# Optimization experiments

Measured on AMD Instinct MI355X. Metric: run time of the kernel, lower is better.

Reference implementation:

```python
import jax, jax.numpy as jnp
import numpy as np

B, P, D, V = 8192, 32, 128, 100000  # batch, max path len, embed dim, label_num


def setup_inputs() -> dict:
    key = jax.random.key(0)
    k1, k2, k3, k4, k5, k6 = jax.random.split(key, 6)
    return {
        "hidden_": jax.random.normal(k1, (B, D), dtype=jnp.float32),
        "target": jax.random.randint(k2, (B,), 0, V, dtype=jnp.int64),
        "target_path": jax.random.randint(k3, (B, P), 0, V, dtype=jnp.int64),
        "target_path_len": jax.random.randint(k4, (B,), 1, P, dtype=jnp.int64),
        "target_code": jax.random.randint(k5, (B, P), 0, 2, dtype=jnp.int64),
        "embed_table": jax.random.normal(k6, (V, D), dtype=jnp.float32) * 0.02,
    }


def reference(hidden_, target, target_path, target_path_len, target_code, embed_table):
    # embeds: [B, P, D] gather of tree-node vectors along each label's path
    embeds = embed_table[target_path]
    # per-node score: sigmoid(<node_vec, hidden>) -> [B, P]
    score = jax.nn.sigmoid(jnp.einsum("bpd,bd->bp", embeds, hidden_))
    flag = target_code.astype(jnp.float32)
    # BCE-style per-node loss, exactly as the TF code writes it
    loss = -jnp.log(flag * score + (1.0 - flag) * (1.0 - score))
    # ragged path mask: positions < target_path_len are valid (tf.ragged.range + batch_gather)
    mask = (jnp.arange(P)[None, :] < target_path_len[:, None]).astype(jnp.float32)
    # reduce_mean over the ragged tensor = sum of valid losses / total valid count
    return jnp.sum(loss * mask) / jnp.sum(mask)
```

## Files before the change

### kernel.cpp

```cpp
#include <hip/hip_runtime.h>

#define BB 8192
#define PP 32
#define DD 128

__global__ __launch_bounds__(256) void hs_loss_kernel(
    const float* __restrict__ hidden,
    const int*   __restrict__ path,
    const int*   __restrict__ path_len,
    const int*   __restrict__ code,
    const float* __restrict__ embed,
    float2* __restrict__ partials)
{
    const int tid = threadIdx.x;
    const int b   = blockIdx.x;
    const int hw  = tid >> 5;
    const int hl  = tid & 31;
    const int p0  = hw * 4;

    const int len = path_len[b];

    float acc = 0.0f;
    if (p0 < len) {
        const int4 idx4 = ((const int4*)(path + b * PP))[hw];
        const int4 cd4  = ((const int4*)(code + b * PP))[hw];
        const float4 h  = ((const float4*)(hidden + (size_t)b * DD))[hl];

        const int nv = min(len - p0, 4);
        const int idx[4] = {idx4.x, idx4.y, idx4.z, idx4.w};
        const int cd[4]  = {cd4.x, cd4.y, cd4.z, cd4.w};

        float4 e[4];
        #pragma unroll
        for (int j = 0; j < 4; ++j)
            if (j < nv) e[j] = ((const float4*)(embed + (size_t)idx[j] * DD))[hl];

        #pragma unroll
        for (int j = 0; j < 4; ++j) {
            if (j < nv) {
                float dot = h.x * e[j].x + h.y * e[j].y + h.z * e[j].z + h.w * e[j].w;
                dot += __shfl_xor(dot, 1);
                dot += __shfl_xor(dot, 2);
                dot += __shfl_xor(dot, 4);
                dot += __shfl_xor(dot, 8);
                dot += __shfl_xor(dot, 16);
                const float z = cd[j] ? -dot : dot;
                acc += fmaxf(z, 0.0f) + log1pf(__expf(-fabsf(z)));
            }
        }
    }

    __shared__ float s_loss[8];
    if (hl == 0) s_loss[hw] = acc;
    __syncthreads();

    if (tid == 0) {
        float v = 0.0f;
        #pragma unroll
        for (int k = 0; k < 8; ++k) v += s_loss[k];
        partials[b] = make_float2(v, (float)len);
    }
}

__global__ __launch_bounds__(1024) void hs_finalize_kernel(
    const float2* __restrict__ partials, float* __restrict__ out)
{
    const int tid = threadIdx.x;
    float ls = 0.0f, cs = 0.0f;
    #pragma unroll
    for (int k = 0; k < BB / 1024; ++k) {
        const float2 v = partials[tid + k * 1024];
        ls += v.x;
        cs += v.y;
    }
    #pragma unroll
    for (int m = 1; m <= 32; m <<= 1) {
        ls += __shfl_xor(ls, m);
        cs += __shfl_xor(cs, m);
    }
    __shared__ float s_l[16], s_c[16];
    const int wave = tid >> 6;
    if ((tid & 63) == 0) { s_l[wave] = ls; s_c[wave] = cs; }
    __syncthreads();
    if (tid == 0) {
        float L = 0.0f, C = 0.0f;
        #pragma unroll
        for (int w = 0; w < 16; ++w) { L += s_l[w]; C += s_c[w]; }
        out[0] = L / C;
    }
}

extern "C" void kernel_launch(void* const* d_in, const int* in_sizes, int n_in,
                              void* d_out, int out_size, void* d_ws, size_t ws_size,
                              hipStream_t stream) {
    const float* hidden   = (const float*)d_in[0];
    const int*   path     = (const int*)d_in[2];
    const int*   path_len = (const int*)d_in[3];
    const int*   code     = (const int*)d_in[4];
    const float* embed    = (const float*)d_in[5];
    float*  out      = (float*)d_out;
    float2* partials = (float2*)d_ws;

    hs_loss_kernel<<<BB, 256, 0, stream>>>(hidden, path, path_len, code,
                                           embed, partials);
    hs_finalize_kernel<<<1, 1024, 0, stream>>>(partials, out);
}
```

Measured before the change: 114.9 us.

## Map one thread per path node and pack eight batch rows per block

Work is remapped so each thread handles one path node and computes the full 128-wide dot product serially. Each block now covers eight batch rows, with the hidden vectors staged in shared memory. This removes the per-node cross-lane shuffle reductions and cuts the block count by eight, which also shrinks the finalize pass to a single load per thread. The cost is that every thread now reads a full embedding row, so the gather loads within a wave are no longer coalesced, and lanes past the path length sit idle.

```diff
diff --git a/kernel.cpp b/kernel.cpp
--- a/kernel.cpp
+++ b/kernel.cpp
@@ -3,6 +3,7 @@
 #define BB 8192
 #define PP 32
 #define DD 128
+#define RPB 8
 
 __global__ __launch_bounds__(256) void hs_loss_kernel(
     const float* __restrict__ hidden,
@@ -13,52 +14,57 @@
     float2* __restrict__ partials)
 {
     const int tid = threadIdx.x;
-    const int b   = blockIdx.x;
-    const int hw  = tid >> 5;
-    const int hl  = tid & 31;
-    const int p0  = hw * 4;
+    const int p   = tid & 31;
+    const int bl  = tid >> 5;
+    const int b   = blockIdx.x * RPB + bl;
 
-    const int len = path_len[b];
+    __shared__ float hlds[RPB * DD];
+    ((float4*)hlds)[tid] = ((const float4*)hidden)[b * (DD / 4) + p];
 
-    float acc = 0.0f;
-    if (p0 < len) {
-        const int4 idx4 = ((const int4*)(path + b * PP))[hw];
-        const int4 cd4  = ((const int4*)(code + b * PP))[hw];
-        const float4 h  = ((const float4*)(hidden + (size_t)b * DD))[hl];
+    const int  len   = path_len[b];
+    const bool valid = (p < len);
 
-        const int nv = min(len - p0, 4);
-        const int idx[4] = {idx4.x, idx4.y, idx4.z, idx4.w};
-        const int cd[4]  = {cd4.x, cd4.y, cd4.z, cd4.w};
+    __syncthreads();
 
-        float4 e[4];
+    float loss = 0.0f;
+    if (valid) {
+        const int idx = path[b * PP + p];
+        const int cd  = code[b * PP + p];
+        const float4* __restrict__ erow = (const float4*)(embed + (size_t)idx * DD);
+        const float4* __restrict__ hrow = (const float4*)(hlds + bl * DD);
+
+        float acc = 0.0f;
         #pragma unroll
-        for (int j = 0; j < 4; ++j)
-            if (j < nv) e[j] = ((const float4*)(embed + (size_t)idx[j] * DD))[hl];
-
-        #pragma unroll
-        for (int j = 0; j < 4; ++j) {
-            if (j < nv) {
-                float dot = h.x * e[j].x + h.y * e[j].y + h.z * e[j].z + h.w * e[j].w;
-                dot += __shfl_xor(dot, 1);
-                dot += __shfl_xor(dot, 2);
-                dot += __shfl_xor(dot, 4);
-                dot += __shfl_xor(dot, 8);
-                dot += __shfl_xor(dot, 16);
-                const float z = cd[j] ? -dot : dot;
-                acc += fmaxf(z, 0.0f) + log1pf(__expf(-fabsf(z)));
+        for (int c0 = 0; c0 < DD / 4; c0 += 8) {
+            float4 e[8];
+            #pragma unroll
+            for (int j = 0; j < 8; ++j) e[j] = erow[c0 + j];
+            #pragma unroll
+            for (int j = 0; j < 8; ++j) {
+                const float4 h = hrow[c0 + j];
+                acc += e[j].x * h.x + e[j].y * h.y
+                     + e[j].z * h.z + e[j].w * h.w;
             }
         }
+        const float z = cd ? -acc : acc;
+        loss = fmaxf(z, 0.0f) + __logf(1.0f + __expf(-fabsf(z)));
     }
 
-    __shared__ float s_loss[8];
-    if (hl == 0) s_loss[hw] = acc;
+    const unsigned long long bal = __ballot(valid);
+
+    #pragma unroll
+    for (int m = 1; m <= 32; m <<= 1) loss += __shfl_xor(loss, m);
+
+    __shared__ float s_l[4], s_c[4];
+    const int wv = tid >> 6;
+    if ((tid & 63) == 0) {
+        s_l[wv] = loss;
+        s_c[wv] = (float)__popcll(bal);
+    }
     __syncthreads();
-
     if (tid == 0) {
-        float v = 0.0f;
-        #pragma unroll
-        for (int k = 0; k < 8; ++k) v += s_loss[k];
-        partials[b] = make_float2(v, (float)len);
+        partials[blockIdx.x] = make_float2(s_l[0] + s_l[1] + s_l[2] + s_l[3],
+                                           s_c[0] + s_c[1] + s_c[2] + s_c[3]);
     }
 }
 
@@ -66,13 +72,8 @@
     const float2* __restrict__ partials, float* __restrict__ out)
 {
     const int tid = threadIdx.x;
-    float ls = 0.0f, cs = 0.0f;
-    #pragma unroll
-    for (int k = 0; k < BB / 1024; ++k) {
-        const float2 v = partials[tid + k * 1024];
-        ls += v.x;
-        cs += v.y;
-    }
+    const float2 v = partials[tid];
+    float ls = v.x, cs = v.y;
     #pragma unroll
     for (int m = 1; m <= 32; m <<= 1) {
         ls += __shfl_xor(ls, m);
@@ -101,7 +102,7 @@
     float*  out      = (float*)d_out;
     float2* partials = (float2*)d_ws;
 
-    hs_loss_kernel<<<BB, 256, 0, stream>>>(hidden, path, path_len, code,
-                                           embed, partials);
+    hs_loss_kernel<<<BB / RPB, 256, 0, stream>>>(hidden, path, path_len, code,
+                                                 embed, partials);
     hs_finalize_kernel<<<1, 1024, 0, stream>>>(partials, out);
 }
```

New measurement: 108.4 us. 1.06x faster.
